# Optimization experiments

Hardware: AMD Instinct MI355X
Metric: run time of the kernel (lower is better)

Reference implementation:

```python
import jax, jax.numpy as jnp
import numpy as np

N = 6144      # num_sample / nodes per graph
E = 196608    # edges per graph (avg degree 32)
F = 256       # input feature dim (same for all 4 graphs)
H = 256       # hidden_channels (== F so all SAGEConv layers are HxH)
D = 512       # fusion dim (hardcoded in module)
G = 4         # number of graphs
ATT = 128     # attention bottleneck (hardcoded)
WS = 0.05     # weight init scale


def setup_inputs() -> dict:
    key = jax.random.key(0)
    k = jax.random.split(key, 16)
    return {
        "xs": jax.random.normal(k[0], (G, N, F), jnp.float32),
        "edge_index": jax.random.randint(k[1], (G, 2, E), 0, N),
        "x_content": jax.random.normal(k[2], (N, F), jnp.float32),
        # SAGEConv params: per graph, 3 layers, lin_l (with bias) on aggregated
        # neighbors, lin_r (no bias) on root. F == H so all layers stack.
        "sage_Wl": jax.random.normal(k[3], (G, 3, H, H), jnp.float32) * WS,
        "sage_bl": jnp.zeros((G, 3, H), jnp.float32),
        "sage_Wr": jax.random.normal(k[4], (G, 3, H, H), jnp.float32) * WS,
        # lin1..lin4 : F -> 512
        "lin_W": jax.random.normal(k[5], (G, D, F), jnp.float32) * WS,
        "lin_b": jnp.zeros((G, D), jnp.float32),
        # ResidualFusion attention MLP 512 -> 128 -> 1, softmax over graph axis
        "att_W1": jax.random.normal(k[6], (ATT, D), jnp.float32) * WS,
        "att_b1": jnp.zeros((ATT,), jnp.float32),
        "att_W2": jax.random.normal(k[7], (1, ATT), jnp.float32) * WS,
        "att_b2": jnp.zeros((1,), jnp.float32),
        "res_W": jax.random.normal(k[8], (D, D), jnp.float32) * WS,
        "res_b": jnp.zeros((D,), jnp.float32),
        "fusion_weight": jnp.array([0.7, 0.3], jnp.float32),
        # SelfExpression coefficients, init 1e-8 * ones as in the module
        "C_content": jnp.full((N, N), 1e-8, jnp.float32),
        "C_structure": jnp.full((N, N), 1e-8, jnp.float32),
    }


def _gnn(x, ei, Wl, bl, Wr):
    # One GraphSAGE stack: 3 SAGEConv(mean) layers, relu after each,
    # dropout is identity in eval mode.
    src, dst = ei[0], ei[1]
    deg = jax.ops.segment_sum(jnp.ones((E,), x.dtype), dst, num_segments=N)
    deg = jnp.maximum(deg, 1.0)[:, None]
    for i in range(3):
        m = jax.ops.segment_sum(x[src], dst, num_segments=N) / deg  # mean aggr
        x = jax.nn.relu(m @ Wl[i].T + bl[i] + x @ Wr[i].T)
    return x


def reference(xs, edge_index, x_content, sage_Wl, sage_bl, sage_Wr,
              lin_W, lin_b, att_W1, att_b1, att_W2, att_b2,
              res_W, res_b, fusion_weight, C_content, C_structure):
    # Four GraphSAGE stacks, vmapped over the graph axis.
    xg = jax.vmap(_gnn)(xs, edge_index, sage_Wl, sage_bl, sage_Wr)  # [G,N,F]
    # lin1..lin4 -> [G,N,D]
    feats = jnp.einsum('gnf,gdf->gnd', xg, lin_W) + lin_b[:, None, :]
    # ResidualFusion: attention over stacked features, softmax over graph axis
    h = jax.nn.relu(jnp.einsum('gnd,kd->gnk', feats, att_W1) + att_b1)
    logits = jnp.einsum('gnk,ok->gno', h, att_W2) + att_b2  # [G,N,1]
    w = jax.nn.softmax(logits, axis=0)
    weighted = jnp.sum(w * feats, axis=0)            # [N,D]
    residual = feats[0] @ res_W.T + res_b            # [N,D]
    structure_features = jax.nn.relu(weighted + residual)
    # Coefficient fusion with softmax-normalized scalar weights
    fw = jax.nn.softmax(fusion_weight)
    fusion_expression = fw[0] * C_content + fw[1] * C_structure  # [N,N]
    return (fusion_expression, x_content, structure_features, C_content, C_structure)
```

## Files before the change

### kernel.cpp

```cpp
#include <hip/hip_runtime.h>
#include <hip/hip_bf16.h>

constexpr int N_ = 6144;
constexpr int E_ = 196608;
constexpr int F_ = 256;
constexpr int D_ = 512;
constexpr int G_ = 4;
constexpr int A_ = 128;

typedef short bf16x8 __attribute__((ext_vector_type(8)));
typedef float f32x4 __attribute__((ext_vector_type(4)));
typedef float f4 __attribute__((ext_vector_type(4)));
typedef __hip_bfloat16 hb;

__device__ inline float b2f(unsigned short u) {
    union { unsigned u32; float f; } x; x.u32 = ((unsigned)u) << 16; return x.f;
}
__device__ inline unsigned short f2bu(float f) {
    hb b = __float2bfloat16(f);
    return *reinterpret_cast<unsigned short*>(&b);
}

#define GLD_LDS16(gp, lp) \
    __builtin_amdgcn_global_load_lds((const __attribute__((address_space(1))) void*)(gp), \
                                     (__attribute__((address_space(3))) void*)(lp), 16, 0, 0)

struct SP {
    const f4* Cc; const f4* Cs; const float* fw;
    f4* o0; f4* o3; f4* o4;
    long ib; long ie; int nsb;
};

__device__ void stream_slice(const SP sp, int sb)
{
    float fa = sp.fw[0], fb = sp.fw[1];
    float mx = fmaxf(fa, fb);
    float ea = expf(fa - mx), eb = expf(fb - mx);
    float w0 = ea / (ea + eb), w1 = eb / (ea + eb);
    const long S = (long)sp.nsb * blockDim.x;
    long i = sp.ib + (long)sb * blockDim.x + threadIdx.x;
    for (; i + 3 * S < sp.ie; i += 4 * S) {
        f4 a0 = __builtin_nontemporal_load(sp.Cc + i);
        f4 b0 = __builtin_nontemporal_load(sp.Cs + i);
        f4 a1 = __builtin_nontemporal_load(sp.Cc + i + S);
        f4 b1 = __builtin_nontemporal_load(sp.Cs + i + S);
        f4 a2 = __builtin_nontemporal_load(sp.Cc + i + 2 * S);
        f4 b2 = __builtin_nontemporal_load(sp.Cs + i + 2 * S);
        f4 a3 = __builtin_nontemporal_load(sp.Cc + i + 3 * S);
        f4 b3 = __builtin_nontemporal_load(sp.Cs + i + 3 * S);
        __builtin_nontemporal_store(a0, sp.o3 + i);
        __builtin_nontemporal_store(b0, sp.o4 + i);
        __builtin_nontemporal_store(w0 * a0 + w1 * b0, sp.o0 + i);
        __builtin_nontemporal_store(a1, sp.o3 + i + S);
        __builtin_nontemporal_store(b1, sp.o4 + i + S);
        __builtin_nontemporal_store(w0 * a1 + w1 * b1, sp.o0 + i + S);
        __builtin_nontemporal_store(a2, sp.o3 + i + 2 * S);
        __builtin_nontemporal_store(b2, sp.o4 + i + 2 * S);
        __builtin_nontemporal_store(w0 * a2 + w1 * b2, sp.o0 + i + 2 * S);
        __builtin_nontemporal_store(a3, sp.o3 + i + 3 * S);
        __builtin_nontemporal_store(b3, sp.o4 + i + 3 * S);
        __builtin_nontemporal_store(w0 * a3 + w1 * b3, sp.o0 + i + 3 * S);
    }
    for (; i < sp.ie; i += S) {
        f4 a = __builtin_nontemporal_load(sp.Cc + i);
        f4 b = __builtin_nontemporal_load(sp.Cs + i);
        __builtin_nontemporal_store(a, sp.o3 + i);
        __builtin_nontemporal_store(b, sp.o4 + i);
        __builtin_nontemporal_store(w0 * a + w1 * b, sp.o0 + i);
    }
}

__global__ void k_tail(SP sp) { stream_slice(sp, blockIdx.x); }

__global__ void k_prep(const float* __restrict__ xc, f4* __restrict__ o1,
                       const float* __restrict__ xs, ushort4* __restrict__ xsb,
                       const float* __restrict__ Wl, ushort4* __restrict__ Wlb,
                       const float* __restrict__ Wr, ushort4* __restrict__ Wrb,
                       const float* __restrict__ lin, ushort4* __restrict__ linb,
                       const float* __restrict__ aw, ushort4* __restrict__ awb,
                       const float* __restrict__ rw, ushort4* __restrict__ rwb)
{
    const long n0 = (long)N_ * F_ / 4;
    const long n1 = (long)G_ * N_ * F_ / 4;
    const long n2 = (long)G_ * 3 * F_ * F_ / 4;
    const long n4 = (long)G_ * D_ * F_ / 4;
    const long n5 = (long)A_ * D_ / 4;
    const long n6 = (long)D_ * D_ / 4;
    const long T = n0 + n1 + 2 * n2 + n4 + n5 + n6;
    long stride = (long)gridDim.x * blockDim.x;
    for (long u = (long)blockIdx.x * blockDim.x + threadIdx.x; u < T; u += stride) {
        long v = u;
        if (v < n0) {
            f4 x = __builtin_nontemporal_load((const f4*)xc + v);
            __builtin_nontemporal_store(x, o1 + v);
            continue;
        }
        v -= n0;
        const float* s; ushort4* d;
        if (v < n1) { s = xs; d = xsb; }
        else {
            v -= n1;
            if (v < n2) { s = Wl; d = Wlb; }
            else {
                v -= n2;
                if (v < n2) { s = Wr; d = Wrb; }
                else {
                    v -= n2;
                    if (v < n4) { s = lin; d = linb; }
                    else {
                        v -= n4;
                        if (v < n5) { s = aw; d = awb; }
                        else { v -= n5; s = rw; d = rwb; }
                    }
                }
            }
        }
        f4 x = *((const f4*)s + v);
        ushort4 o;
        o.x = f2bu(x[0]); o.y = f2bu(x[1]); o.z = f2bu(x[2]); o.w = f2bu(x[3]);
        d[v] = o;
    }
}

__global__ void k_count(const int* __restrict__ ei, int* __restrict__ cnt, SP sp)
{
    if ((int)blockIdx.x >= G_ * E_ / 256) { stream_slice(sp, blockIdx.x - G_ * E_ / 256); return; }
    long i = (long)blockIdx.x * blockDim.x + threadIdx.x;
    int g = (int)(i / E_);
    int e = (int)(i % E_);
    int dst = ei[(long)g * 2 * E_ + E_ + e];
    atomicAdd(&cnt[g * N_ + dst], 1);
}

__global__ void k_scan(int* __restrict__ cnt_cursor, int* __restrict__ row_ptr,
                       float* __restrict__ deg, SP sp)
{
    if ((int)blockIdx.x >= G_) { stream_slice(sp, blockIdx.x - G_); return; }
    int g = blockIdx.x;
    __shared__ int sdata[1024];
    __shared__ int s_off;
    if (threadIdx.x == 0) s_off = 0;
    __syncthreads();
    for (int base = 0; base < N_; base += 1024) {
        int idx = g * N_ + base + threadIdx.x;
        int v = cnt_cursor[idx];
        sdata[threadIdx.x] = v;
        __syncthreads();
        for (int d = 1; d < 1024; d <<= 1) {
            int t = (threadIdx.x >= d) ? sdata[threadIdx.x - d] : 0;
            __syncthreads();
            sdata[threadIdx.x] += t;
            __syncthreads();
        }
        int incl = sdata[threadIdx.x];
        int excl = incl - v;
        int rp = s_off + excl;
        row_ptr[g * (N_ + 1) + base + threadIdx.x] = rp;
        cnt_cursor[idx] = rp;
        deg[idx] = (float)(v > 1 ? v : 1);
        __syncthreads();
        if (threadIdx.x == 1023) s_off += incl;
        __syncthreads();
    }
    if (threadIdx.x == 0) row_ptr[g * (N_ + 1) + N_] = s_off;
}

__global__ void k_fill(const int* __restrict__ ei, int* __restrict__ cursor,
                       int* __restrict__ csr_src, SP sp)
{
    if ((int)blockIdx.x >= G_ * E_ / 256) { stream_slice(sp, blockIdx.x - G_ * E_ / 256); return; }
    long i = (long)blockIdx.x * blockDim.x + threadIdx.x;
    int g = (int)(i / E_);
    int e = (int)(i % E_);
    int src = ei[(long)g * 2 * E_ + e];
    int dst = ei[(long)g * 2 * E_ + E_ + e];
    int pos = atomicAdd(&cursor[g * N_ + dst], 1);
    csr_src[(long)g * E_ + pos] = src;
}

__global__ __launch_bounds__(256) void k_aggregate(
    const hb* __restrict__ x, const int* __restrict__ csr_src,
    const int* __restrict__ row_ptr, const float* __restrict__ deg,
    hb* __restrict__ m, SP sp)
{
    int b = blockIdx.x;
    if (b >= G_ * N_ / 4) { stream_slice(sp, b - G_ * N_ / 4); return; }
    int g = (b & 7) >> 1;
    int idx = ((b >> 3) << 1) | (b & 1);
    int node = idx * 4 + (threadIdx.x >> 6);
    int lane = threadIdx.x & 63;
    int qq = lane >> 4;
    int l16 = (lane & 15) * 16;
    const hb* xg = x + (long)g * N_ * F_;
    const int* rp = row_ptr + g * (N_ + 1);
    const int* cs = csr_src + (long)g * E_;
    int s = __builtin_amdgcn_readfirstlane(rp[node]);
    int e = __builtin_amdgcn_readfirstlane(rp[node + 1]);
    float a[16] = {};
    #pragma unroll 2
    for (int j = s; j < e; j += 4) {
        if (j + qq < e) {
            int src = cs[j + qq];
            const bf16x8* p = (const bf16x8*)(xg + (long)src * F_ + l16);
            bf16x8 v0 = p[0], v1 = p[1];
            #pragma unroll
            for (int q = 0; q < 8; ++q) a[q]     += b2f((unsigned short)v0[q]);
            #pragma unroll
            for (int q = 0; q < 8; ++q) a[q + 8] += b2f((unsigned short)v1[q]);
        }
    }
    #pragma unroll
    for (int q = 0; q < 16; ++q) {
        a[q] += __shfl_xor(a[q], 16);
        a[q] += __shfl_xor(a[q], 32);
    }
    if (qq == 0) {
        float inv = 1.0f / deg[g * N_ + node];
        bf16x8 lo, hi;
        #pragma unroll
        for (int q = 0; q < 8; ++q) { lo[q] = (short)f2bu(a[q] * inv); hi[q] = (short)f2bu(a[q + 8] * inv); }
        *(bf16x8*)(m + ((long)g * N_ + node) * F_ + l16) = lo;
        *(bf16x8*)(m + ((long)g * N_ + node) * F_ + l16 + 8) = hi;
    }
}

template <bool DUAL, bool RELU, bool LOGITS, bool FUSEOUT, bool PIN>
__global__ __launch_bounds__(256) void k_mfma_nt(
    const hb* __restrict__ A1, const hb* __restrict__ B1,
    const hb* __restrict__ A2, const hb* __restrict__ B2,
    const float* __restrict__ bias, hb* __restrict__ C,
    int ncols, int nrows, int ng, int Nc, int K,
    long a_batch, long b_batch, long bias_batch, long c_batch,
    const float* __restrict__ W2, const float* __restrict__ b2,
    float* __restrict__ logits,
    const float* __restrict__ lgAll, const hb* __restrict__ fAll,
    float* __restrict__ o2,
    SP sp)
{
    const int nComp = ncols * nrows * ng;
    int b = blockIdx.x;
    if (b >= nComp) { stream_slice(sp, b - nComp); return; }
    int g, col, row;
    if (PIN) {
        g = (b & 7) >> 1;
        int idx = ((b >> 3) << 1) | (b & 1);
        col = idx % ncols; row = idx / ncols;
    } else {
        col = b % ncols;
        int r2 = b / ncols;
        row = r2 % nrows; g = r2 / nrows;
    }
    const int row0 = row * 128;
    const int col0 = col * 128;

    const hb* A1p = A1 + (long)g * a_batch;
    const hb* B1p = B1 + (long)g * b_batch;
    const hb* A2p = nullptr;
    const hb* B2p = nullptr;
    if (DUAL) { A2p = A2 + (long)g * a_batch; B2p = B2 + (long)g * b_batch; }
    const float* biasp = bias + (long)g * bias_batch;
    hb* Cp = C + (long)g * c_batch;

    __shared__ hb As[128 * 64];
    __shared__ hb Bs[128 * 64];
    __shared__ float sLog[2][128];
    __shared__ float sW[128][4];

    const int tid = threadIdx.x;
    const int lane = tid & 63;
    const int wid = tid >> 6;
    const int wr = wid >> 1;
    const int wc = wid & 1;

    if (FUSEOUT) {
        if (tid < 128) {
            int rr = row0 + tid;
            float l0 = lgAll[rr], l1 = lgAll[N_ + rr], l2 = lgAll[2 * N_ + rr], l3 = lgAll[3 * N_ + rr];
            float mx = fmaxf(fmaxf(l0, l1), fmaxf(l2, l3));
            float e0 = expf(l0 - mx), e1 = expf(l1 - mx), e2 = expf(l2 - mx), e3 = expf(l3 - mx);
            float inv = 1.f / (e0 + e1 + e2 + e3);
            sW[tid][0] = e0 * inv; sW[tid][1] = e1 * inv;
            sW[tid][2] = e2 * inv; sW[tid][3] = e3 * inv;
        }
    }

    const int srow = tid >> 3;
    const int sk8  = (tid & 7) * 8;

    f32x4 acc[4][4] = {};

    const int fr  = lane & 15;
    const int fkq = (lane >> 4) * 8;

    const int npass = DUAL ? 2 : 1;
    for (int pass = 0; pass < npass; ++pass) {
        const hb* A = (DUAL && pass) ? A2p : A1p;
        const hb* B = (DUAL && pass) ? B2p : B1p;
        for (int k0 = 0; k0 < K; k0 += 64) {
            __syncthreads();
            #pragma unroll
            for (int c = 0; c < 4; ++c) {
                int r = c * 32 + srow;
                GLD_LDS16(A + (long)(row0 + r) * K + k0 + sk8, As + r * 64 + sk8);
                GLD_LDS16(B + (long)(col0 + r) * K + k0 + sk8, Bs + r * 64 + sk8);
            }
            __syncthreads();

            bf16x8 af[4][2], bfr[4][2];
            #pragma unroll
            for (int m = 0; m < 4; ++m)
                #pragma unroll
                for (int kk = 0; kk < 2; ++kk)
                    af[m][kk] = *(const bf16x8*)(As + (wr * 64 + m * 16 + fr) * 64 + kk * 32 + fkq);
            #pragma unroll
            for (int n = 0; n < 4; ++n)
                #pragma unroll
                for (int kk = 0; kk < 2; ++kk)
                    bfr[n][kk] = *(const bf16x8*)(Bs + (wc * 64 + n * 16 + fr) * 64 + kk * 32 + fkq);

            #pragma unroll
            for (int m = 0; m < 4; ++m)
                #pragma unroll
                for (int n = 0; n < 4; ++n)
                    #pragma unroll
                    for (int kk = 0; kk < 2; ++kk)
                        acc[m][n] = __builtin_amdgcn_mfma_f32_16x16x32_bf16(
                            af[m][kk], bfr[n][kk], acc[m][n], 0, 0, 0);
        }
    }

    const int r4 = (lane >> 4) * 4;
    const int cc = lane & 15;

    if (LOGITS) {
        float w2v[4], bv[4];
        #pragma unroll
        for (int n = 0; n < 4; ++n) {
            int c2 = wc * 64 + n * 16 + cc;
            w2v[n] = W2[c2];
            bv[n]  = biasp[c2];
        }
        #pragma unroll
        for (int m = 0; m < 4; ++m) {
            #pragma unroll
            for (int j = 0; j < 4; ++j) {
                float p = 0.f;
                #pragma unroll
                for (int n = 0; n < 4; ++n) {
                    float h = fmaxf(acc[m][n][j] + bv[n], 0.f);
                    p += h * w2v[n];
                }
                p += __shfl_xor(p, 1); p += __shfl_xor(p, 2);
                p += __shfl_xor(p, 4); p += __shfl_xor(p, 8);
                if (cc == 0) sLog[wc][wr * 64 + m * 16 + r4 + j] = p;
            }
        }
        __syncthreads();
        if (tid < 128)
            logits[(long)g * N_ + row0 + tid] = sLog[0][tid] + sLog[1][tid] + b2[0];
    } else if (FUSEOUT) {
        const unsigned short* fu = (const unsigned short*)fAll;
        #pragma unroll
        for (int m = 0; m < 4; ++m) {
            #pragma unroll
            for (int n = 0; n < 4; ++n) {
                int c2 = col0 + wc * 64 + n * 16 + cc;
                float bv = biasp[c2];
                #pragma unroll
                for (int j = 0; j < 4; ++j) {
                    int rl = wr * 64 + m * 16 + r4 + j;
                    int rr = row0 + rl;
                    float s = acc[m][n][j] + bv;
                    #pragma unroll
                    for (int gg = 0; gg < 4; ++gg)
                        s += sW[rl][gg] * b2f(fu[((long)gg * N_ + rr) * D_ + c2]);
                    __builtin_nontemporal_store(fmaxf(s, 0.f), o2 + (long)rr * D_ + c2);
                }
            }
        }
    } else {
        #pragma unroll
        for (int m = 0; m < 4; ++m) {
            #pragma unroll
            for (int n = 0; n < 4; ++n) {
                int c2 = col0 + wc * 64 + n * 16 + cc;
                float bv = biasp[c2];
                #pragma unroll
                for (int j = 0; j < 4; ++j) {
                    int rr = row0 + wr * 64 + m * 16 + r4 + j;
                    float v = acc[m][n][j] + bv;
                    if (RELU) v = fmaxf(v, 0.f);
                    Cp[(long)rr * Nc + c2] = __float2bfloat16(v);
                }
            }
        }
    }
}

extern "C" void kernel_launch(void* const* d_in, const int* in_sizes, int n_in,
                              void* d_out, int out_size, void* d_ws, size_t ws_size,
                              hipStream_t stream)
{
    const float* xs        = (const float*)d_in[0];
    const int*   ei        = (const int*)  d_in[1];
    const float* x_content = (const float*)d_in[2];
    const float* sage_Wl   = (const float*)d_in[3];
    const float* sage_bl   = (const float*)d_in[4];
    const float* sage_Wr   = (const float*)d_in[5];
    const float* lin_W     = (const float*)d_in[6];
    const float* lin_b     = (const float*)d_in[7];
    const float* att_W1    = (const float*)d_in[8];
    const float* att_b1    = (const float*)d_in[9];
    const float* att_W2    = (const float*)d_in[10];
    const float* att_b2    = (const float*)d_in[11];
    const float* res_W     = (const float*)d_in[12];
    const float* res_b     = (const float*)d_in[13];
    const float* fusion_w  = (const float*)d_in[14];
    const float* Cc        = (const float*)d_in[15];
    const float* Cs        = (const float*)d_in[16];

    float* out0 = (float*)d_out;
    float* out1 = out0 + (size_t)N_ * N_;
    float* out2 = out1 + (size_t)N_ * F_;
    float* out3 = out2 + (size_t)N_ * D_;
    float* out4 = out3 + (size_t)N_ * N_;

    char* w = (char*)d_ws;
    auto alloc = [&](size_t bytes) {
        char* p = w;
        w += (bytes + 255) & ~(size_t)255;
        return p;
    };
    hb* xsb   = (hb*)alloc((size_t)G_ * N_ * F_ * 2);
    hb* xA    = (hb*)alloc((size_t)G_ * N_ * F_ * 2);
    hb* xB    = (hb*)alloc((size_t)G_ * N_ * F_ * 2);
    hb* mb    = (hb*)alloc((size_t)G_ * N_ * F_ * 2);
    hb* feats = (hb*)alloc((size_t)G_ * N_ * D_ * 2);
    hb* Wlb   = (hb*)alloc((size_t)G_ * 3 * F_ * F_ * 2);
    hb* Wrb   = (hb*)alloc((size_t)G_ * 3 * F_ * F_ * 2);
    hb* linWb = (hb*)alloc((size_t)G_ * D_ * F_ * 2);
    hb* attWb = (hb*)alloc((size_t)A_ * D_ * 2);
    hb* resWb = (hb*)alloc((size_t)D_ * D_ * 2);
    float* logit = (float*)alloc((size_t)G_ * N_ * 4);
    float* deg   = (float*)alloc((size_t)G_ * N_ * 4);
    int*   rowp  = (int*)  alloc((size_t)G_ * (N_ + 1) * 4);
    int*   curs  = (int*)  alloc((size_t)G_ * N_ * 4);
    int*   csrc  = (int*)  alloc((size_t)G_ * E_ * 4);

    const long U = (long)N_ * N_ / 4;
    const int cum[13] = {0, 15, 40, 65, 125, 180, 240, 295, 355, 410, 460, 485, 525};
    long B[13];
    for (int i = 0; i < 13; ++i) B[i] = U * cum[i] / 1000;
    const int SB_FLAT = 256;
    const int SB_GEMM = 128;
    const int TAILB   = 2048;
    auto mkSP = [&](int i, int nsb) {
        SP sp;
        sp.Cc = (const f4*)Cc; sp.Cs = (const f4*)Cs; sp.fw = fusion_w;
        sp.o0 = (f4*)out0; sp.o3 = (f4*)out3; sp.o4 = (f4*)out4;
        sp.ib = B[i]; sp.ie = B[i + 1]; sp.nsb = nsb;
        return sp;
    };
    SP tail;
    tail.Cc = (const f4*)Cc; tail.Cs = (const f4*)Cs; tail.fw = fusion_w;
    tail.o0 = (f4*)out0; tail.o3 = (f4*)out3; tail.o4 = (f4*)out4;
    tail.ib = B[12]; tail.ie = U; tail.nsb = TAILB;

    k_prep<<<1024, 256, 0, stream>>>(
        x_content, (f4*)out1, xs, (ushort4*)xsb,
        sage_Wl, (ushort4*)Wlb, sage_Wr, (ushort4*)Wrb,
        lin_W, (ushort4*)linWb, att_W1, (ushort4*)attWb, res_W, (ushort4*)resWb);

    hipMemsetAsync(curs, 0, (size_t)G_ * N_ * 4, stream);
    k_count<<<G_ * E_ / 256 + SB_FLAT, 256, 0, stream>>>(ei, curs, mkSP(0, SB_FLAT));
    k_scan<<<G_ + SB_FLAT, 1024, 0, stream>>>(curs, rowp, deg, mkSP(1, SB_FLAT));
    k_fill<<<G_ * E_ / 256 + SB_FLAT, 256, 0, stream>>>(ei, curs, csrc, mkSP(2, SB_FLAT));

    const hb* xin = xsb;
    hb* xout = xA;
    for (int layer = 0; layer < 3; ++layer) {
        k_aggregate<<<G_ * N_ / 4 + SB_FLAT, 256, 0, stream>>>(
            xin, csrc, rowp, deg, mb, mkSP(3 + 2 * layer, SB_FLAT));
        k_mfma_nt<true, true, false, false, true>
            <<<(F_ / 128) * (N_ / 128) * G_ + SB_GEMM, 256, 0, stream>>>(
            mb, Wlb + (size_t)layer * F_ * F_,
            xin, Wrb + (size_t)layer * F_ * F_,
            sage_bl + (size_t)layer * F_, xout,
            F_ / 128, N_ / 128, G_, F_, F_,
            (long)N_ * F_, (long)3 * F_ * F_, (long)3 * F_, (long)N_ * F_,
            nullptr, nullptr, nullptr, nullptr, nullptr, nullptr,
            mkSP(4 + 2 * layer, SB_GEMM));
        xin = xout;
        xout = (layer == 0) ? xB : xA;
    }
    const hb* xg = xA;

    k_mfma_nt<false, false, false, false, true>
        <<<(D_ / 128) * (N_ / 128) * G_ + SB_GEMM, 256, 0, stream>>>(
        xg, linWb, nullptr, nullptr, lin_b, feats,
        D_ / 128, N_ / 128, G_, D_, F_,
        (long)N_ * F_, (long)D_ * F_, (long)D_, (long)N_ * D_,
        nullptr, nullptr, nullptr, nullptr, nullptr, nullptr,
        mkSP(9, SB_GEMM));

    k_mfma_nt<false, true, true, false, true>
        <<<(A_ / 128) * (N_ / 128) * G_ + SB_GEMM, 256, 0, stream>>>(
        feats, attWb, nullptr, nullptr, att_b1, nullptr,
        A_ / 128, N_ / 128, G_, A_, D_,
        (long)N_ * D_, 0L, 0L, 0L,
        att_W2, att_b2, logit, nullptr, nullptr, nullptr,
        mkSP(10, SB_GEMM));

    k_mfma_nt<false, false, false, true, false>
        <<<(D_ / 128) * (N_ / 128) * 1 + SB_GEMM, 256, 0, stream>>>(
        feats, resWb, nullptr, nullptr, res_b, nullptr,
        D_ / 128, N_ / 128, 1, D_, D_,
        0L, 0L, 0L, 0L,
        nullptr, nullptr, nullptr, logit, feats, out2,
        mkSP(11, SB_GEMM));

    k_tail<<<TAILB, 256, 0, stream>>>(tail);
}
```

Measured before the change: 462.8 us.

## Fold curs memset into prep kernel and rebalance co-scheduled stream slices

Removes the separate memset by zeroing the edge-count cursors inside the prep kernel. The prep kernel also gains extra blocks that stream a slice of the N×N coefficient fusion, so that copy overlaps prep work. The split of the big streaming job across kernels is retuned: more goes to the small attention and residual GEMMs, whose grids are tiny, and less to the final tail kernel. The risk is that the streaming blocks compete for bandwidth with the main work in each kernel.

```diff
diff --git a/kernel.cpp b/kernel.cpp
--- a/kernel.cpp
+++ b/kernel.cpp
@@ -11,6 +11,7 @@
 typedef short bf16x8 __attribute__((ext_vector_type(8)));
 typedef float f32x4 __attribute__((ext_vector_type(4)));
 typedef float f4 __attribute__((ext_vector_type(4)));
+typedef int i4 __attribute__((ext_vector_type(4)));
 typedef __hip_bfloat16 hb;
 
 __device__ inline float b2f(unsigned short u) {
@@ -78,18 +79,23 @@
                        const float* __restrict__ Wr, ushort4* __restrict__ Wrb,
                        const float* __restrict__ lin, ushort4* __restrict__ linb,
                        const float* __restrict__ aw, ushort4* __restrict__ awb,
-                       const float* __restrict__ rw, ushort4* __restrict__ rwb)
-{
+                       const float* __restrict__ rw, ushort4* __restrict__ rwb,
+                       i4* __restrict__ cursz, int PB, SP sp)
+{
+    if ((int)blockIdx.x >= PB) { stream_slice(sp, blockIdx.x - PB); return; }
+    const long nz = (long)G_ * N_ / 4;
     const long n0 = (long)N_ * F_ / 4;
     const long n1 = (long)G_ * N_ * F_ / 4;
     const long n2 = (long)G_ * 3 * F_ * F_ / 4;
     const long n4 = (long)G_ * D_ * F_ / 4;
     const long n5 = (long)A_ * D_ / 4;
     const long n6 = (long)D_ * D_ / 4;
-    const long T = n0 + n1 + 2 * n2 + n4 + n5 + n6;
-    long stride = (long)gridDim.x * blockDim.x;
+    const long T = nz + n0 + n1 + 2 * n2 + n4 + n5 + n6;
+    long stride = (long)PB * blockDim.x;
     for (long u = (long)blockIdx.x * blockDim.x + threadIdx.x; u < T; u += stride) {
         long v = u;
+        if (v < nz) { cursz[v] = i4{0, 0, 0, 0}; continue; }
+        v -= nz;
         if (v < n0) {
             f4 x = __builtin_nontemporal_load((const f4*)xc + v);
             __builtin_nontemporal_store(x, o1 + v);
@@ -448,39 +454,40 @@
     int*   csrc  = (int*)  alloc((size_t)G_ * E_ * 4);
 
     const long U = (long)N_ * N_ / 4;
-    const int cum[13] = {0, 15, 40, 65, 125, 180, 240, 295, 355, 410, 460, 485, 525};
-    long B[13];
-    for (int i = 0; i < 13; ++i) B[i] = U * cum[i] / 1000;
+    const int cum[14] = {0, 100, 115, 123, 143, 183, 233, 273, 323, 363, 413, 468, 648, 898};
+    long B[14];
+    for (int i = 0; i < 14; ++i) B[i] = U * cum[i] / 1000;
+    const int PREPB   = 512;
+    const int SB_PREP = 512;
     const int SB_FLAT = 256;
-    const int SB_GEMM = 128;
-    const int TAILB   = 2048;
+    const int SB_GEMM = 256;
+    const int SB_ATT  = 768;
+    const int SB_RES  = 1024;
+    const int TAILB   = 1024;
     auto mkSP = [&](int i, int nsb) {
         SP sp;
         sp.Cc = (const f4*)Cc; sp.Cs = (const f4*)Cs; sp.fw = fusion_w;
         sp.o0 = (f4*)out0; sp.o3 = (f4*)out3; sp.o4 = (f4*)out4;
-        sp.ib = B[i]; sp.ie = B[i + 1]; sp.nsb = nsb;
+        sp.ib = B[i]; sp.ie = (i == 13) ? U : B[i + 1]; sp.nsb = nsb;
         return sp;
     };
-    SP tail;
-    tail.Cc = (const f4*)Cc; tail.Cs = (const f4*)Cs; tail.fw = fusion_w;
-    tail.o0 = (f4*)out0; tail.o3 = (f4*)out3; tail.o4 = (f4*)out4;
-    tail.ib = B[12]; tail.ie = U; tail.nsb = TAILB;
-
-    k_prep<<<1024, 256, 0, stream>>>(
+    SP tail = mkSP(13, TAILB);
+
+    k_prep<<<PREPB + SB_PREP, 256, 0, stream>>>(
         x_content, (f4*)out1, xs, (ushort4*)xsb,
         sage_Wl, (ushort4*)Wlb, sage_Wr, (ushort4*)Wrb,
-        lin_W, (ushort4*)linWb, att_W1, (ushort4*)attWb, res_W, (ushort4*)resWb);
-
-    hipMemsetAsync(curs, 0, (size_t)G_ * N_ * 4, stream);
-    k_count<<<G_ * E_ / 256 + SB_FLAT, 256, 0, stream>>>(ei, curs, mkSP(0, SB_FLAT));
-    k_scan<<<G_ + SB_FLAT, 1024, 0, stream>>>(curs, rowp, deg, mkSP(1, SB_FLAT));
-    k_fill<<<G_ * E_ / 256 + SB_FLAT, 256, 0, stream>>>(ei, curs, csrc, mkSP(2, SB_FLAT));
+        lin_W, (ushort4*)linWb, att_W1, (ushort4*)attWb, res_W, (ushort4*)resWb,
+        (i4*)curs, PREPB, mkSP(0, SB_PREP));
+
+    k_count<<<G_ * E_ / 256 + SB_FLAT, 256, 0, stream>>>(ei, curs, mkSP(1, SB_FLAT));
+    k_scan<<<G_ + SB_FLAT, 1024, 0, stream>>>(curs, rowp, deg, mkSP(2, SB_FLAT));
+    k_fill<<<G_ * E_ / 256 + SB_FLAT, 256, 0, stream>>>(ei, curs, csrc, mkSP(3, SB_FLAT));
 
     const hb* xin = xsb;
     hb* xout = xA;
     for (int layer = 0; layer < 3; ++layer) {
         k_aggregate<<<G_ * N_ / 4 + SB_FLAT, 256, 0, stream>>>(
-            xin, csrc, rowp, deg, mb, mkSP(3 + 2 * layer, SB_FLAT));
+            xin, csrc, rowp, deg, mb, mkSP(4 + 2 * layer, SB_FLAT));
         k_mfma_nt<true, true, false, false, true>
             <<<(F_ / 128) * (N_ / 128) * G_ + SB_GEMM, 256, 0, stream>>>(
             mb, Wlb + (size_t)layer * F_ * F_,
@@ -489,7 +496,7 @@
             F_ / 128, N_ / 128, G_, F_, F_,
             (long)N_ * F_, (long)3 * F_ * F_, (long)3 * F_, (long)N_ * F_,
             nullptr, nullptr, nullptr, nullptr, nullptr, nullptr,
-            mkSP(4 + 2 * layer, SB_GEMM));
+            mkSP(5 + 2 * layer, SB_GEMM));
         xin = xout;
         xout = (layer == 0) ? xB : xA;
     }
@@ -501,23 +508,23 @@
         D_ / 128, N_ / 128, G_, D_, F_,
         (long)N_ * F_, (long)D_ * F_, (long)D_, (long)N_ * D_,
         nullptr, nullptr, nullptr, nullptr, nullptr, nullptr,
-        mkSP(9, SB_GEMM));
+        mkSP(10, SB_GEMM));
 
     k_mfma_nt<false, true, true, false, true>
-        <<<(A_ / 128) * (N_ / 128) * G_ + SB_GEMM, 256, 0, stream>>>(
+        <<<(A_ / 128) * (N_ / 128) * G_ + SB_ATT, 256, 0, stream>>>(
         feats, attWb, nullptr, nullptr, att_b1, nullptr,
         A_ / 128, N_ / 128, G_, A_, D_,
         (long)N_ * D_, 0L, 0L, 0L,
         att_W2, att_b2, logit, nullptr, nullptr, nullptr,
-        mkSP(10, SB_GEMM));
+        mkSP(11, SB_ATT));
 
     k_mfma_nt<false, false, false, true, false>
-        <<<(D_ / 128) * (N_ / 128) * 1 + SB_GEMM, 256, 0, stream>>>(
+        <<<(D_ / 128) * (N_ / 128) * 1 + SB_RES, 256, 0, stream>>>(
         feats, resWb, nullptr, nullptr, res_b, nullptr,
         D_ / 128, N_ / 128, 1, D_, D_,
         0L, 0L, 0L, 0L,
         nullptr, nullptr, nullptr, logit, feats, out2,
-        mkSP(11, SB_GEMM));
+        mkSP(12, SB_RES));
 
     k_tail<<<TAILB, 256, 0, stream>>>(tail);
 }
```

Measured after the change: 433.9 us. -6.2%, faster.
